# Optimization experiments

Measured on AMD Instinct MI355X. Metric: run time of the kernel, lower is better.

Reference implementation:

```python
import jax, jax.numpy as jnp
import numpy as np
import math
from jax import lax

B, L_IN, D_MODEL = 128, 1000, 384
SEQ = 250          # AdaptiveMaxPool1d target length
NHEAD, NL = 8, 4
HID = 342          # convolution_hidden_dim
NUM_CLASSES = 10
FACTOR = 5         # ProbAttention factor


def _ln(x, w, b, eps=1e-5):
    mu = x.mean(-1, keepdims=True)
    var = ((x - mu) ** 2).mean(-1, keepdims=True)
    return (x - mu) * lax.rsqrt(var + eps) * w + b


def _conv1d(x, w, b, groups):
    # x: [B,C,L], w: [O, I/groups, K], SAME padding (padding=1 for k=3)
    y = lax.conv_general_dilated(x, w, (1,), 'SAME',
                                 dimension_numbers=('NCH', 'OIH', 'NCH'),
                                 feature_group_count=groups)
    return y + b[None, :, None]


def _prob_attention(x, Wq, bq, Wk, bk, Wv, bv, Wo, bo, key):
    # Informer-style ProbSparse attention, mask_flag=False, eval mode (no dropout)
    Bs, L, d = x.shape
    H, Dh = NHEAD, d // NHEAD
    q = (x @ Wq + bq).reshape(Bs, L, H, Dh).transpose(0, 2, 1, 3)  # [B,H,L,Dh]
    k = (x @ Wk + bk).reshape(Bs, L, H, Dh).transpose(0, 2, 1, 3)
    v = (x @ Wv + bv).reshape(Bs, L, H, Dh).transpose(0, 2, 1, 3)
    U = min(int(FACTOR * math.ceil(math.log(L))), L)  # sampled keys per query (=30)
    u = min(int(FACTOR * math.ceil(math.log(L))), L)  # top queries kept (=30)
    idx = jax.random.randint(key, (L, U), 0, L)        # shared key sample per query row
    k_samp = k[:, :, idx, :]                            # [B,H,L,U,Dh] gather
    qk_samp = jnp.einsum('bhld,bhlud->bhlu', q, k_samp)
    M = qk_samp.max(-1) - qk_samp.mean(-1)              # sparsity measure [B,H,L]
    top = lax.top_k(M, u)[1]                            # [B,H,u]
    q_red = jnp.take_along_axis(q, top[..., None], axis=2)          # [B,H,u,Dh]
    scores = jnp.einsum('bhud,bhld->bhul', q_red, k) / math.sqrt(Dh)
    attn = jax.nn.softmax(scores, axis=-1)
    ctx_top = jnp.einsum('bhul,bhld->bhud', attn, v)                # [B,H,u,Dh]
    # initial context = mean of V (mask_flag=False); scatter top-query contexts
    ctx = jnp.broadcast_to(v.mean(2, keepdims=True), (Bs, H, L, Dh))
    bi = jnp.arange(Bs)[:, None, None]
    hi = jnp.arange(H)[None, :, None]
    ctx = ctx.at[bi, hi, top].set(ctx_top)
    out = ctx.transpose(0, 2, 1, 3).reshape(Bs, L, d)
    return out @ Wo + bo


def _forward(x, pos_embed, ln_in_w, ln_in_b, lnA_w, lnA_b, Wq, bq, Wk, bk, Wv, bv,
             Wo, bo, lnB_w, lnB_b, c1a_w, c1a_b, c1b_w, c1b_b, lnC_w, lnC_b,
             c2_w, c2_b, ln2_w, ln2_b, fc_w, fc_b):
    Bs, Lin, d = x.shape
    # AdaptiveMaxPool1d(250): Lin=1000 is an exact multiple -> window-4 max
    x = x.reshape(Bs, SEQ, Lin // SEQ, d).max(axis=2)
    x = _ln(x, ln_in_w, ln_in_b)
    x = x + pos_embed[:, :SEQ, :]                       # positional embedding (dropout off)
    for l in range(NL):
        key = jax.random.fold_in(jax.random.key(42), l)
        # residual 1: LN -> ProbSparse attention
        h = _ln(x, lnA_w[l], lnA_b[l])
        x = x + _prob_attention(h, Wq[l], bq[l], Wk[l], bk[l], Wv[l], bv[l],
                                Wo[l], bo[l], key)
        # residual 2: LN -> grouped conv over sequence axis (channels = d_model)
        h = _ln(x, lnB_w[l], lnB_b[l]).transpose(0, 2, 1)  # [B,d,L]
        h = jax.nn.gelu(_conv1d(h, c1a_w[l], c1a_b[l], 3))
        h = _conv1d(h, c1b_w[l], c1b_b[l], 3)
        x = x + h.transpose(0, 2, 1)
        # residual 3: LN -> grouped conv treating sequence (250) as channels
        h = _ln(x, lnC_w[l], lnC_b[l])                     # [B,250,d]
        h = jax.nn.gelu(_conv1d(h, c2_w[l], c2_b[l], 2))
        x = x + h
    x = _ln(x, ln2_w, ln2_b)
    x = x.max(axis=1)                                   # AdaptiveMaxPool1d(1)
    x = _ln(x, ln2_w, ln2_b)                            # LN2 reused, per original
    return x @ fc_w + fc_b


def setup_inputs() -> dict:
    key = jax.random.key(0)
    ks = jax.random.split(key, 12)
    s = 0.02
    f32 = jnp.float32
    inp = {
        'x': jax.random.normal(ks[0], (B, L_IN, D_MODEL), f32),
        'pos_embed': jax.random.normal(ks[1], (1, 1500, D_MODEL), f32) * s,
        'ln_in_w': jnp.ones((D_MODEL,), f32), 'ln_in_b': jnp.zeros((D_MODEL,), f32),
        'lnA_w': jnp.ones((NL, D_MODEL), f32), 'lnA_b': jnp.zeros((NL, D_MODEL), f32),
        'Wq': jax.random.normal(ks[2], (NL, D_MODEL, D_MODEL), f32) * s,
        'bq': jnp.zeros((NL, D_MODEL), f32),
        'Wk': jax.random.normal(ks[3], (NL, D_MODEL, D_MODEL), f32) * s,
        'bk': jnp.zeros((NL, D_MODEL), f32),
        'Wv': jax.random.normal(ks[4], (NL, D_MODEL, D_MODEL), f32) * s,
        'bv': jnp.zeros((NL, D_MODEL), f32),
        'Wo': jax.random.normal(ks[5], (NL, D_MODEL, D_MODEL), f32) * s,
        'bo': jnp.zeros((NL, D_MODEL), f32),
        'lnB_w': jnp.ones((NL, D_MODEL), f32), 'lnB_b': jnp.zeros((NL, D_MODEL), f32),
        'c1a_w': jax.random.normal(ks[6], (NL, HID, D_MODEL // 3, 3), f32) * s,
        'c1a_b': jnp.zeros((NL, HID), f32),
        'c1b_w': jax.random.normal(ks[7], (NL, D_MODEL, HID // 3, 3), f32) * s,
        'c1b_b': jnp.zeros((NL, D_MODEL), f32),
        'lnC_w': jnp.ones((NL, D_MODEL), f32), 'lnC_b': jnp.zeros((NL, D_MODEL), f32),
        'c2_w': jax.random.normal(ks[8], (NL, SEQ, SEQ // 2, 3), f32) * s,
        'c2_b': jnp.zeros((NL, SEQ), f32),
        'ln2_w': jnp.ones((D_MODEL,), f32), 'ln2_b': jnp.zeros((D_MODEL,), f32),
        'fc_w': jax.random.normal(ks[9], (D_MODEL, NUM_CLASSES), f32) * s,
        'fc_b': jnp.zeros((NUM_CLASSES,), f32),
    }
    return inp


def reference(x, pos_embed, ln_in_w, ln_in_b, lnA_w, lnA_b, Wq, bq, Wk, bk, Wv, bv,
              Wo, bo, lnB_w, lnB_b, c1a_w, c1a_b, c1b_w, c1b_b, lnC_w, lnC_b,
              c2_w, c2_b, ln2_w, ln2_b, fc_w, fc_b):
    return _forward(x, pos_embed, ln_in_w, ln_in_b, lnA_w, lnA_b, Wq, bq, Wk, bk,
                    Wv, bv, Wo, bo, lnB_w, lnB_b, c1a_w, c1a_b, c1b_w, c1b_b,
                    lnC_w, lnC_b, c2_w, c2_b, ln2_w, ln2_b, fc_w, fc_b)
```

## Files before the change

### kernel.cpp

```cpp
#include <hip/hip_runtime.h>
#include <hip/hip_bf16.h>
#include <cfloat>
#include <cstdint>

static constexpr int Bb   = 128;
static constexpr int SEQ  = 250;
static constexpr int DM   = 384;
static constexpr int NH   = 8;
static constexpr int DHd  = 48;
static constexpr int HID  = 342;
static constexpr int UU   = 30;

using bf16 = __hip_bfloat16;
typedef __attribute__((ext_vector_type(8))) short bf16x8;
typedef __attribute__((ext_vector_type(4))) float f32x4;

__device__ __forceinline__ float unpk_lo(uint32_t p){ return __builtin_bit_cast(float, p << 16); }
__device__ __forceinline__ float unpk_hi(uint32_t p){ return __builtin_bit_cast(float, p & 0xffff0000u); }

__device__ __forceinline__ int swz_st(int lane){ return (((lane & 7) ^ (lane >> 3)) << 3); }
__device__ __forceinline__ int swz_rd(int ks, int lane){ return ((((ks<<2) + (lane >> 4)) ^ (lane & 7)) << 3); }

__device__ __forceinline__ int xcd_swz(int orig, int nwg){
  int q = nwg >> 3, r = nwg & 7;
  int x = orig & 7, i = orig >> 3;
  int start = (x < r) ? x*(q+1) : r*(q+1) + (x-r)*q;
  return start + i;
}

__device__ __forceinline__ uint32_t rotl32(uint32_t x, int n){ return (x<<n)|(x>>(32-n)); }
#define TF_R(x0,x1,r) { x0 += x1; x1 = rotl32(x1,(r)); x1 ^= x0; }
__device__ inline void threefry(uint32_t k0, uint32_t k1, uint32_t x0, uint32_t x1,
                                uint32_t &o0, uint32_t &o1){
  uint32_t ks2 = k0 ^ k1 ^ 0x1BD11BDAu;
  x0 += k0; x1 += k1;
  TF_R(x0,x1,13) TF_R(x0,x1,15) TF_R(x0,x1,26) TF_R(x0,x1,6)
  x0 += k1; x1 += ks2 + 1u;
  TF_R(x0,x1,17) TF_R(x0,x1,29) TF_R(x0,x1,16) TF_R(x0,x1,24)
  x0 += ks2; x1 += k0 + 2u;
  TF_R(x0,x1,13) TF_R(x0,x1,15) TF_R(x0,x1,26) TF_R(x0,x1,6)
  x0 += k0; x1 += k1 + 3u;
  TF_R(x0,x1,17) TF_R(x0,x1,29) TF_R(x0,x1,16) TF_R(x0,x1,24)
  x0 += k1; x1 += ks2 + 4u;
  TF_R(x0,x1,13) TF_R(x0,x1,15) TF_R(x0,x1,26) TF_R(x0,x1,6)
  x0 += ks2; x1 += k0 + 5u;
  o0 = x0; o1 = x1;
}

__global__ void idx_kernel(int* __restrict__ IDX){
  int i = blockIdx.x*256 + threadIdx.x;
  if (i >= 4*7500) return;
  int l = i / 7500;
  int t = i % 7500;
  uint32_t fk0, fk1;
  threefry(0u, 42u, 0u, (uint32_t)l, fk0, fk1);
  uint32_t a0,a1,b0,b1;
  threefry(fk0, fk1, 0u, 2u, a0, a1);
  threefry(fk0, fk1, 1u, 3u, b0, b1);
  uint32_t c0 = (t < 3750) ? (uint32_t)t          : (uint32_t)(t-3750);
  uint32_t c1 = (t < 3750) ? (uint32_t)(t+3750)   : (uint32_t)t;
  uint32_t y0, y1, hi, lo;
  threefry(a0, b0, c0, c1, y0, y1); hi = (t < 3750) ? y0 : y1;
  threefry(a1, b1, c0, c1, y0, y1); lo = (t < 3750) ? y0 : y1;
  uint32_t val = ((hi % 250u) * 46u + (lo % 250u)) % 250u;
  IDX[i] = (int)val;
}

__device__ __forceinline__ float block_sum(float v, float* red){
  v += __shfl_down(v,32); v += __shfl_down(v,16); v += __shfl_down(v,8);
  v += __shfl_down(v,4);  v += __shfl_down(v,2);  v += __shfl_down(v,1);
  int lane = threadIdx.x & 63, wid = threadIdx.x >> 6, nw = blockDim.x >> 6;
  __syncthreads();
  if (lane == 0) red[wid] = v;
  __syncthreads();
  float r = red[0];
  for (int i=1;i<nw;i++) r += red[i];
  return r;
}

__device__ __forceinline__ float gelu_tanh(float x){
  float t = 0.7978845608028654f * (x + 0.044715f * x * x * x);
  return 0.5f * x * (1.f + tanhf(t));
}

__global__ __launch_bounds__(384) void pool_ln_pos(const float* __restrict__ xin,
    const float* __restrict__ pos, const float* __restrict__ w, const float* __restrict__ b,
    float* __restrict__ X){
  __shared__ float red[8];
  int bs = blockIdx.x; int bb = bs / SEQ, s = bs % SEQ; int d = threadIdx.x;
  const float* xp = xin + ((size_t)bb*1000 + (size_t)s*4)*DM + d;
  float v = fmaxf(fmaxf(xp[0], xp[DM]), fmaxf(xp[2*DM], xp[3*DM]));
  float mu = block_sum(v, red) * (1.f/DM);
  float diff = v - mu;
  float var = block_sum(diff*diff, red) * (1.f/DM);
  X[(size_t)bs*DM + d] = diff * rsqrtf(var + 1e-5f) * w[d] + b[d] + pos[(size_t)s*DM + d];
}

template<int MODE>
__global__ __launch_bounds__(256) void ln_wave(const float* __restrict__ in,
    float* __restrict__ o32, bf16* __restrict__ o16, bf16* __restrict__ olo,
    const float* __restrict__ w, const float* __restrict__ b){
  size_t row = (size_t)blockIdx.x*4 + (threadIdx.x >> 6);
  int lane = threadIdx.x & 63;
  const float* rp = in + row*DM;
  float v[6];
  #pragma unroll
  for (int i = 0; i < 6; i++) v[i] = rp[lane + 64*i];
  float s = v[0]+v[1]+v[2]+v[3]+v[4]+v[5];
  #pragma unroll
  for (int off = 32; off; off >>= 1) s += __shfl_xor(s, off);
  float mu = s * (1.f/DM);
  float q = 0.f;
  #pragma unroll
  for (int i = 0; i < 6; i++){ float d = v[i]-mu; q += d*d; }
  #pragma unroll
  for (int off = 32; off; off >>= 1) q += __shfl_xor(q, off);
  float rs = rsqrtf(q*(1.f/DM) + 1e-5f);
  #pragma unroll
  for (int i = 0; i < 6; i++){
    int d = lane + 64*i;
    float y = (v[i]-mu)*rs*w[d] + b[d];
    if (MODE == 0) o32[row*DM + d] = y;
    if (MODE == 1) o16[row*DM + d] = __float2bfloat16(y);
    if (MODE == 2){
      bf16 h = __float2bfloat16(y);
      o16[row*DM + d] = h;
      olo[row*DM + d] = __float2bfloat16(y - __bfloat162float(h));
    }
  }
}

__device__ __forceinline__ void gload16(const void* g, void* l){
  __builtin_amdgcn_global_load_lds(
      (__attribute__((address_space(1))) void*)(g),
      (__attribute__((address_space(3))) void*)(l), 16, 0, 0);
}

template<int EPI>
__global__ __launch_bounds__(256) void mfma_gemm(
    const bf16* __restrict__ A, const bf16* __restrict__ WT,
    const float* __restrict__ bias, float* __restrict__ Cf, bf16* __restrict__ Cb,
    const bf16* __restrict__ zpage)
{
  __shared__ bf16 As[128*64];
  __shared__ bf16 Bs[128*64];
  const int tid = threadIdx.x;
  const int wid = tid >> 6, lane = tid & 63;
  const int wr = wid >> 1, wc = wid & 1;
  const int wg = xcd_swz(blockIdx.x, 750);
  const int bm = (wg / 3) * 128;
  const int bn = (wg % 3) * 128;
  const int srow = lane >> 3;
  const int scolz = swz_st(lane);

  f32x4 acc[4][4] = {};
  for (int ck = 0; ck < 6; ck++){
    const int kk0 = ck * 64;
    __syncthreads();
    #pragma unroll
    for (int s = 0; s < 4; s++){
      int row = wid*32 + s*8 + srow;
      gload16(A + (size_t)(bm + row)*DM + kk0 + scolz, &As[(wid*32 + s*8)*64]);
    }
    #pragma unroll
    for (int s = 0; s < 4; s++){
      int row = wid*32 + s*8 + srow;
      gload16(WT + (size_t)(bn + row)*DM + kk0 + scolz, &Bs[(wid*32 + s*8)*64]);
    }
    __syncthreads();
    #pragma unroll
    for (int ks = 0; ks < 2; ks++){
      const int fo = swz_rd(ks, lane);
      bf16x8 af[4], bg[4];
      #pragma unroll
      for (int m = 0; m < 4; m++)
        af[m] = *(const bf16x8*)&As[(wr*64 + m*16 + (lane & 15))*64 + fo];
      #pragma unroll
      for (int n = 0; n < 4; n++)
        bg[n] = *(const bf16x8*)&Bs[(wc*64 + n*16 + (lane & 15))*64 + fo];
      #pragma unroll
      for (int m = 0; m < 4; m++)
        #pragma unroll
        for (int n = 0; n < 4; n++)
          acc[m][n] = __builtin_amdgcn_mfma_f32_16x16x32_bf16(af[m], bg[n], acc[m][n], 0, 0, 0);
    }
  }
  const int c_l = lane & 15, r4 = (lane >> 4) * 4;
  #pragma unroll
  for (int m = 0; m < 4; m++){
    #pragma unroll
    for (int n = 0; n < 4; n++){
      #pragma unroll
      for (int r = 0; r < 4; r++){
        int token = bm + wr*64 + m*16 + r4 + r;
        int col   = bn + wc*64 + n*16 + c_l;
        float v = acc[m][n][r] + bias[col];
        if (EPI == 0)      Cf[(size_t)token*DM + col] = v;
        else if (EPI == 1) Cf[(size_t)token*DM + col] += v;
        else if (EPI == 2) Cb[(size_t)token*DM + col] = __float2bfloat16(gelu_tanh(v));
        else               Cb[(size_t)token*DM + col] = __float2bfloat16(v);
      }
    }
  }
}

template<int EPI, int KIN>
__global__ __launch_bounds__(256) void mfma_c1g(
    const bf16* __restrict__ A, const bf16* __restrict__ WG,
    const float* __restrict__ bias, float* __restrict__ Cf, bf16* __restrict__ Cb,
    const bf16* __restrict__ zpage)
{
  __shared__ bf16 As[128*64];
  __shared__ bf16 Bs[128*64];
  const int tid = threadIdx.x;
  const int wid = tid >> 6, lane = tid & 63;
  const int wr = wid >> 1, wc = wid & 1;
  const int wg = xcd_swz(blockIdx.x, 750);
  const int bm = (wg / 3) * 128;
  const int g  = wg % 3;
  const int srow = lane >> 3;
  const int scolz = swz_st(lane);

  f32x4 acc[4][4] = {};
  for (int ck = 0; ck < 6; ck++){
    const int tap = ck >> 1;
    const int kk0 = (ck & 1) * 64;
    __syncthreads();
    #pragma unroll
    for (int s = 0; s < 4; s++){
      int row = wid*32 + s*8 + srow;
      int token = bm + row;
      int l = token - (token/SEQ)*SEQ;
      int ls = l + tap - 1;
      bool valid = (ls >= 0) && (ls < SEQ);
      const bf16* src = valid ? (A + (size_t)(token + tap - 1)*DM + g*KIN + kk0 + scolz) : zpage;
      gload16(src, &As[(wid*32 + s*8)*64]);
    }
    #pragma unroll
    for (int s = 0; s < 4; s++){
      int row = wid*32 + s*8 + srow;
      gload16(WG + ((size_t)(g*3 + tap)*128 + row)*128 + kk0 + scolz, &Bs[(wid*32 + s*8)*64]);
    }
    __syncthreads();
    #pragma unroll
    for (int ks = 0; ks < 2; ks++){
      const int fo = swz_rd(ks, lane);
      bf16x8 af[4], bg[4];
      #pragma unroll
      for (int m = 0; m < 4; m++)
        af[m] = *(const bf16x8*)&As[(wr*64 + m*16 + (lane & 15))*64 + fo];
      #pragma unroll
      for (int n = 0; n < 4; n++)
        bg[n] = *(const bf16x8*)&Bs[(wc*64 + n*16 + (lane & 15))*64 + fo];
      #pragma unroll
      for (int m = 0; m < 4; m++)
        #pragma unroll
        for (int n = 0; n < 4; n++)
          acc[m][n] = __builtin_amdgcn_mfma_f32_16x16x32_bf16(af[m], bg[n], acc[m][n], 0, 0, 0);
    }
  }
  const int c_l = lane & 15, r4 = (lane >> 4) * 4;
  #pragma unroll
  for (int m = 0; m < 4; m++){
    #pragma unroll
    for (int n = 0; n < 4; n++){
      #pragma unroll
      for (int r = 0; r < 4; r++){
        int token = bm + wr*64 + m*16 + r4 + r;
        int cl    = wc*64 + n*16 + c_l;
        if (EPI == 2){
          if (cl < 114){
            int col = g*114 + cl;
            float v = acc[m][n][r] + bias[col];
            Cb[(size_t)token*DM + col] = __float2bfloat16(gelu_tanh(v));
          }
        } else {
          int col = g*128 + cl;
          float v = acc[m][n][r] + bias[col];
          Cf[(size_t)token*DM + col] += v;
        }
      }
    }
  }
}

__global__ __launch_bounds__(256) void mfma_qk2(
    const bf16* __restrict__ Ahi, const bf16* __restrict__ Alo,
    const bf16* __restrict__ WqT, const bf16* __restrict__ WkT,
    const float* __restrict__ bq, const float* __restrict__ bk,
    bf16* __restrict__ Qhi, bf16* __restrict__ Qlo,
    bf16* __restrict__ Khi, bf16* __restrict__ Klo)
{
  __shared__ bf16 As[128*64];
  __shared__ bf16 BsQ[64*64];
  __shared__ bf16 BsK[64*64];
  const int tid = threadIdx.x;
  const int wid = tid >> 6, lane = tid & 63;
  const int wr = wid >> 1, wc = wid & 1;
  const int wg = xcd_swz(blockIdx.x, 1500);
  const int bm = (wg / 6) * 128;
  const int bn = (wg % 6) * 64;
  const int srow = lane >> 3;
  const int scolz = swz_st(lane);

  f32x4 accQ[4][2] = {};
  f32x4 accK[4][2] = {};
  for (int kk6 = 0; kk6 < 6; kk6++){
    const int kk0 = kk6 * 64;
    for (int p = 0; p < 3; p++){
      const size_t wo = (p == 1) ? (size_t)DM*DM : 0;
      __syncthreads();
      if (p != 1){
        const bf16* Asrc = (p == 0) ? Ahi : Alo;
        #pragma unroll
        for (int s = 0; s < 4; s++){
          int row = wid*32 + s*8 + srow;
          gload16(Asrc + (size_t)(bm + row)*DM + kk0 + scolz, &As[(wid*32 + s*8)*64]);
        }
      }
      #pragma unroll
      for (int s = 0; s < 2; s++){
        int row = wid*16 + s*8 + srow;
        gload16(WqT + wo + (size_t)(bn + row)*DM + kk0 + scolz, &BsQ[(wid*16 + s*8)*64]);
        gload16(WkT + wo + (size_t)(bn + row)*DM + kk0 + scolz, &BsK[(wid*16 + s*8)*64]);
      }
      __syncthreads();
      #pragma unroll
      for (int ks = 0; ks < 2; ks++){
        const int fo = swz_rd(ks, lane);
        bf16x8 af[4], bgq[2], bgk[2];
        #pragma unroll
        for (int m = 0; m < 4; m++)
          af[m] = *(const bf16x8*)&As[(wr*64 + m*16 + (lane & 15))*64 + fo];
        #pragma unroll
        for (int n = 0; n < 2; n++){
          bgq[n] = *(const bf16x8*)&BsQ[(wc*32 + n*16 + (lane & 15))*64 + fo];
          bgk[n] = *(const bf16x8*)&BsK[(wc*32 + n*16 + (lane & 15))*64 + fo];
        }
        #pragma unroll
        for (int m = 0; m < 4; m++)
          #pragma unroll
          for (int n = 0; n < 2; n++){
            accQ[m][n] = __builtin_amdgcn_mfma_f32_16x16x32_bf16(af[m], bgq[n], accQ[m][n], 0, 0, 0);
            accK[m][n] = __builtin_amdgcn_mfma_f32_16x16x32_bf16(af[m], bgk[n], accK[m][n], 0, 0, 0);
          }
      }
    }
  }
  const int c_l = lane & 15, r4 = (lane >> 4) * 4;
  #pragma unroll
  for (int m = 0; m < 4; m++)
    #pragma unroll
    for (int n = 0; n < 2; n++)
      #pragma unroll
      for (int r = 0; r < 4; r++){
        int token = bm + wr*64 + m*16 + r4 + r;
        int col   = bn + wc*32 + n*16 + c_l;
        size_t off = (size_t)token*DM + col;
        float qv = accQ[m][n][r] + bq[col];
        float kv = accK[m][n][r] + bk[col];
        bf16 qh = __float2bfloat16(qv);
        bf16 kh = __float2bfloat16(kv);
        Qhi[off] = qh; Qlo[off] = __float2bfloat16(qv - __bfloat162float(qh));
        Khi[off] = kh; Klo[off] = __float2bfloat16(kv - __bfloat162float(kh));
      }
}

__global__ __launch_bounds__(256) void conv2_mfma(
    const bf16* __restrict__ HT, const bf16* __restrict__ W2T,
    const float* __restrict__ bias, float* __restrict__ X,
    const bf16* __restrict__ zpage)
{
  __shared__ bf16 As[128*64];
  __shared__ bf16 Bs[128*64];
  const int tid = threadIdx.x;
  const int wid = tid >> 6, lane = tid & 63;
  const int wr = wid >> 1, wc = wid & 1;
  const int wg = xcd_swz(blockIdx.x, 768);
  const int bn = (wg % 3) * 128;
  const int g  = (wg / 3) & 1;
  const int b  = wg / 6;
  const int srow = lane >> 3;
  const int scolz = swz_st(lane);
  const bf16* Wbase = W2T + (size_t)g*3*128*128;

  f32x4 acc[4][4] = {};
  for (int ck = 0; ck < 6; ck++){
    const int tap = ck >> 1;
    const int kk0 = (ck & 1) * 64;
    __syncthreads();
    #pragma unroll
    for (int s = 0; s < 4; s++){
      gload16(Wbase + ((size_t)tap*128 + wid*32 + s*8 + srow)*128 + kk0 + scolz, &As[(wid*32 + s*8)*64]);
    }
    #pragma unroll
    for (int s = 0; s < 4; s++){
      int row = wid*32 + s*8 + srow;
      int sd = bn + row + tap - 1;
      const bf16* src = (sd >= 0 && sd < DM)
        ? (HT + (((size_t)b*DM + sd)*2 + g)*128 + kk0 + scolz) : zpage;
      gload16(src, &Bs[(wid*32 + s*8)*64]);
    }
    __syncthreads();
    #pragma unroll
    for (int ks = 0; ks < 2; ks++){
      const int fo = swz_rd(ks, lane);
      bf16x8 af[4], bg[4];
      #pragma unroll
      for (int m = 0; m < 4; m++)
        af[m] = *(const bf16x8*)&As[(wr*64 + m*16 + (lane & 15))*64 + fo];
      #pragma unroll
      for (int n = 0; n < 4; n++)
        bg[n] = *(const bf16x8*)&Bs[(wc*64 + n*16 + (lane & 15))*64 + fo];
      #pragma unroll
      for (int m = 0; m < 4; m++)
        #pragma unroll
        for (int n = 0; n < 4; n++)
          acc[m][n] = __builtin_amdgcn_mfma_f32_16x16x32_bf16(af[m], bg[n], acc[m][n], 0, 0, 0);
    }
  }
  const int c_l = lane & 15, r4 = (lane >> 4) * 4;
  #pragma unroll
  for (int m = 0; m < 4; m++){
    #pragma unroll
    for (int n = 0; n < 4; n++){
      #pragma unroll
      for (int r = 0; r < 4; r++){
        int lo = wr*64 + m*16 + r4 + r;
        if (lo < 125){
          int d = bn + wc*64 + n*16 + c_l;
          float v = acc[m][n][r] + bias[g*125 + lo];
          X[((size_t)b*SEQ + g*125 + lo)*DM + d] += gelu_tanh(v);
        }
      }
    }
  }
}

__global__ __launch_bounds__(256) void transpose_ht(const bf16* __restrict__ H,
                                                    bf16* __restrict__ HT){
  __shared__ bf16 t[68][66];
  int d0 = blockIdx.x * 64;
  int p0 = blockIdx.y * 64;
  int b  = blockIdx.z;
  int tid = threadIdx.x;
  int l0 = p0 - 3;
  for (int i = tid; i < 68*64; i += 256){
    int r = i >> 6, c = i & 63;
    int l = l0 + r;
    bf16 v = __float2bfloat16(0.f);
    if (l >= 0 && l < SEQ) v = H[((size_t)b*SEQ + l)*DM + d0 + c];
    t[r][c] = v;
  }
  __syncthreads();
  for (int i = tid; i < 64*64; i += 256){
    int rr = i >> 6, cc = i & 63;
    int p = p0 + cc;
    int gg = p >> 7, li = p & 127;
    int l = gg*125 + li;
    bf16 v = __float2bfloat16(0.f);
    if (li < 125 && l < SEQ) v = t[l - l0][rr];
    HT[((size_t)b*DM + d0 + rr)*256 + p] = v;
  }
}

__global__ void zfill(bf16* z){ z[threadIdx.x] = __float2bfloat16(0.f); }

__global__ __launch_bounds__(256) void build_projT(const float* __restrict__ Wv,
    const float* __restrict__ Wo, bf16* __restrict__ WvT, bf16* __restrict__ WoT){
  __shared__ float t[32][33];
  int mat = blockIdx.z;
  const float* W = (mat < 4) ? (Wv + (size_t)mat*DM*DM) : (Wo + (size_t)(mat-4)*DM*DM);
  bf16* WT = (mat < 4) ? (WvT + (size_t)mat*DM*DM) : (WoT + (size_t)(mat-4)*DM*DM);
  int k0 = blockIdx.y*32, n0 = blockIdx.x*32;
  int tx = threadIdx.x & 31, ty = threadIdx.x >> 5;
  #pragma unroll
  for (int r = 0; r < 32; r += 8)
    t[ty + r][tx] = W[(size_t)(k0 + ty + r)*DM + n0 + tx];
  __syncthreads();
  #pragma unroll
  for (int r = 0; r < 32; r += 8)
    WT[(size_t)(n0 + ty + r)*DM + k0 + tx] = __float2bfloat16(t[tx][ty + r]);
}

__global__ __launch_bounds__(256) void build_qkhl(const float* __restrict__ Wq,
    const float* __restrict__ Wk, bf16* __restrict__ WT){
  __shared__ float t[32][33];
  int mat = blockIdx.z;
  const float* W = (mat < 4) ? (Wq + (size_t)mat*DM*DM) : (Wk + (size_t)(mat-4)*DM*DM);
  bf16* hi = WT + (size_t)mat*2*DM*DM;
  bf16* lo = hi + (size_t)DM*DM;
  int k0 = blockIdx.y*32, n0 = blockIdx.x*32;
  int tx = threadIdx.x & 31, ty = threadIdx.x >> 5;
  #pragma unroll
  for (int r = 0; r < 32; r += 8)
    t[ty + r][tx] = W[(size_t)(k0 + ty + r)*DM + n0 + tx];
  __syncthreads();
  #pragma unroll
  for (int r = 0; r < 32; r += 8){
    float w = t[tx][ty + r];
    bf16 h = __float2bfloat16(w);
    hi[(size_t)(n0 + ty + r)*DM + k0 + tx] = h;
    lo[(size_t)(n0 + ty + r)*DM + k0 + tx] = __float2bfloat16(w - __bfloat162float(h));
  }
}

__global__ void build_biasA(const float* __restrict__ bin, float* __restrict__ bias_pad){
  int i = blockIdx.x*256 + threadIdx.x;
  if (i >= 4*DM) return;
  int l = i/DM, n = i%DM;
  bias_pad[i] = (n < HID) ? bin[l*HID + n] : 0.f;
}

__global__ void build_c1aG(const float* __restrict__ W, bf16* __restrict__ WG){
  int i = blockIdx.x*256 + threadIdx.x;
  if (i >= 4*3*3*128*128) return;
  int k   = i & 127;
  int n   = (i >> 7) & 127;
  int tap = (i / 16384) % 3;
  int g   = (i / 49152) % 3;
  int l   = i / 147456;
  float v = 0.f;
  if (n < 114)
    v = W[(((size_t)l*HID + g*114 + n)*128 + k)*3 + tap];
  WG[i] = __float2bfloat16(v);
}

__global__ void build_c1bG(const float* __restrict__ W, bf16* __restrict__ WG){
  int i = blockIdx.x*256 + threadIdx.x;
  if (i >= 4*3*3*128*128) return;
  int k   = i & 127;
  int n   = (i >> 7) & 127;
  int tap = (i / 16384) % 3;
  int g   = (i / 49152) % 3;
  int l   = i / 147456;
  float v = 0.f;
  if (k < 114)
    v = W[(((size_t)l*DM + g*128 + n)*114 + k)*3 + tap];
  WG[i] = __float2bfloat16(v);
}

__global__ void build_c2T(const float* __restrict__ W, bf16* __restrict__ WT){
  int i = blockIdx.x*256 + threadIdx.x;
  if (i >= 4*2*3*128*128) return;
  int li = i & 127;
  int lo = (i >> 7) & 127;
  int t  = (i / 16384) % 3;
  int g  = (i / 49152) % 2;
  int l  = i / 98304;
  float v = 0.f;
  if (lo < 125 && li < 125)
    v = W[(((size_t)l*SEQ + g*125 + lo)*125 + li)*3 + t];
  WT[i] = __float2bfloat16(v);
}

__global__ __launch_bounds__(256) void probe_mfma(
    const bf16* __restrict__ Qhi, const bf16* __restrict__ Qlo,
    const bf16* __restrict__ Khi, const bf16* __restrict__ Klo,
    const int* __restrict__ idx, int* __restrict__ TOP,
    const bf16* __restrict__ zpage)
{
  __shared__ bf16  Qsh[32*64];
  __shared__ bf16  Qsl[32*64];
  __shared__ float Ssh[32*257];
  __shared__ int   IDXsh[32*UU];
  __shared__ float Msh[256];
  __shared__ float s_redv[4];
  __shared__ int   s_redi[4];
  __shared__ int   s_win;
  const int bh = xcd_swz(blockIdx.x, Bb*NH);
  const int h = bh & 7; const int b = bh >> 3;
  const int tid = threadIdx.x;
  const int wid = tid >> 6, lane = tid & 63;
  const int scolz = swz_st(lane);
  const size_t qkbase = (size_t)(b*SEQ)*DM + h*DHd;

  bf16x8 kfh[4][2] = {};
  bf16x8 kfl[4][2] = {};
  {
    const int colb = wid*64 + (lane & 15);
    const int kb   = (lane >> 4) * 8;
    #pragma unroll
    for (int n = 0; n < 4; n++){
      int col = colb + n*16;
      int cc  = (col < SEQ) ? col : (SEQ-1);
      const bf16* ph = Khi + qkbase + (size_t)cc*DM;
      const bf16* pl = Klo + qkbase + (size_t)cc*DM;
      kfh[n][0] = *(const bf16x8*)(ph + kb);
      kfl[n][0] = *(const bf16x8*)(pl + kb);
      if (kb + 32 < DHd){
        kfh[n][1] = *(const bf16x8*)(ph + kb + 32);
        kfl[n][1] = *(const bf16x8*)(pl + kb + 32);
      }
    }
  }

  const int c_l = lane & 15, r4 = (lane >> 4) * 4;
  for (int t = 0; t < 8; t++){
    const int r0 = t*32;
    {
      int row = r0 + wid*8 + (lane >> 3);
      bool v = (row < SEQ) && (scolz < DHd);
      const bf16* sh = v ? (Qhi + qkbase + (size_t)row*DM + scolz) : zpage;
      const bf16* sl = v ? (Qlo + qkbase + (size_t)row*DM + scolz) : zpage;
      gload16(sh, &Qsh[(wid*8)*64]);
      gload16(sl, &Qsl[(wid*8)*64]);
    }
    for (int i = tid; i < 32*UU; i += 256){
      int r = i / UU;
      int row = r0 + r;
      IDXsh[i] = (row < SEQ) ? idx[row*UU + (i - r*UU)] : 0;
    }
    __syncthreads();
    f32x4 acc[2][4] = {};
    #pragma unroll
    for (int p = 0; p < 3; p++){
      const bf16* A = (p < 2) ? Qsh : Qsl;
      #pragma unroll
      for (int ks = 0; ks < 2; ks++){
        const int fo = swz_rd(ks, lane);
        bf16x8 af[2];
        #pragma unroll
        for (int m = 0; m < 2; m++)
          af[m] = *(const bf16x8*)&A[(m*16 + (lane & 15))*64 + fo];
        #pragma unroll
        for (int m = 0; m < 2; m++)
          #pragma unroll
          for (int n = 0; n < 4; n++){
            bf16x8 bg = (p == 1) ? kfl[n][ks] : kfh[n][ks];
            acc[m][n] = __builtin_amdgcn_mfma_f32_16x16x32_bf16(af[m], bg, acc[m][n], 0, 0, 0);
          }
      }
    }
    #pragma unroll
    for (int m = 0; m < 2; m++)
      #pragma unroll
      for (int n = 0; n < 4; n++)
        #pragma unroll
        for (int r = 0; r < 4; r++)
          Ssh[(m*16 + r4 + r)*257 + wid*64 + n*16 + c_l] = acc[m][n][r];
    __syncthreads();
    {
      int rl = tid >> 3, s8 = tid & 7;
      int row = r0 + rl;
      float mx = -FLT_MAX, sm = 0.f;
      #pragma unroll
      for (int uu = 0; uu < 4; uu++){
        int u = s8 + uu*8;
        if (u < UU){
          int c = IDXsh[rl*UU + u];
          float v = Ssh[rl*257 + c];
          mx = fmaxf(mx, v); sm += v;
        }
      }
      #pragma unroll
      for (int off = 4; off; off >>= 1){
        mx = fmaxf(mx, __shfl_xor(mx, off));
        sm += __shfl_xor(sm, off);
      }
      if (s8 == 0 && row < SEQ) Msh[row] = mx - sm*(1.f/UU);
    }
    __syncthreads();
  }
  float Mv  = (tid < SEQ) ? Msh[tid] : -FLT_MAX;
  int  myid = (tid < SEQ) ? tid : (1<<30);
  for (int sel = 0; sel < UU; sel++){
    float bv = Mv; int bi = myid;
    #pragma unroll
    for (int off = 32; off; off >>= 1){
      float ov = __shfl_xor(bv, off);
      int   oi = __shfl_xor(bi, off);
      if (ov > bv || (ov == bv && oi < bi)){ bv = ov; bi = oi; }
    }
    if (lane == 0){ s_redv[wid] = bv; s_redi[wid] = bi; }
    __syncthreads();
    if (tid == 0){
      float wv = s_redv[0]; int wi = s_redi[0];
      #pragma unroll
      for (int q = 1; q < 4; q++)
        if (s_redv[q] > wv || (s_redv[q] == wv && s_redi[q] < wi)){ wv = s_redv[q]; wi = s_redi[q]; }
      TOP[(size_t)bh*UU + sel] = wi;
      s_win = wi;
    }
    __syncthreads();
    if (myid == s_win) Mv = -FLT_MAX;
  }
}

static constexpr int SSTR = 260;
static constexpr int VSTR = 132;
__global__ __launch_bounds__(256) void attn_ctx5(
    const bf16* __restrict__ Qhi, const bf16* __restrict__ Qlo,
    const bf16* __restrict__ Khi, const bf16* __restrict__ Klo,
    const bf16* __restrict__ V16,
    const int* __restrict__ TOP, bf16* __restrict__ CTX,
    const bf16* __restrict__ zpage)
{
  __shared__ bf16  Qt[32*64];
  __shared__ bf16  Qtl[32*64];
  __shared__ float Ssh[32*SSTR];
  __shared__ uint32_t Vsh[DHd*VSTR];
  __shared__ float vpart[5][DHd];
  __shared__ float vmean[DHd];
  __shared__ float invsh[32];
  __shared__ int   TOPsh[32];
  __shared__ int   mark[SEQ];
  const int bh = xcd_swz(blockIdx.x, Bb*NH);
  const int h = bh & 7; const int b = bh >> 3;
  const int tid = threadIdx.x;
  const int wid = tid >> 6, lane = tid & 63;
  const int scolz = swz_st(lane);
  const size_t base = (size_t)(b*SEQ)*DM + h*DHd;

  bf16x8 kfh[4][2] = {};
  bf16x8 kfl[4][2] = {};
  {
    const int colb = wid*64 + (lane & 15);
    const int kb   = (lane >> 4) * 8;
    #pragma unroll
    for (int n = 0; n < 4; n++){
      int col = colb + n*16;
      int cc  = (col < SEQ) ? col : (SEQ-1);
      const bf16* ph = Khi + base + (size_t)cc*DM;
      const bf16* pl = Klo + base + (size_t)cc*DM;
      kfh[n][0] = *(const bf16x8*)(ph + kb);
      kfl[n][0] = *(const bf16x8*)(pl + kb);
      if (kb + 32 < DHd){
        kfh[n][1] = *(const bf16x8*)(ph + kb + 32);
        kfl[n][1] = *(const bf16x8*)(pl + kb + 32);
      }
    }
  }
  if (tid < UU) TOPsh[tid] = TOP[(size_t)bh*UU + tid];
  for (int i = tid; i < SEQ; i += 256) mark[i] = -1;
  const uint16_t* vp16 = (const uint16_t*)(V16 + base);
  for (int i = tid; i < DHd*128; i += 256){
    int dh = i >> 7, jp = i & 127;
    uint32_t v = 0;
    if (jp < 125){
      uint32_t a = vp16[(size_t)(2*jp)*DM + dh];
      uint32_t c = vp16[(size_t)(2*jp+1)*DM + dh];
      v = a | (c << 16);
    }
    Vsh[dh*VSTR + jp] = v;
  }
  {
    int row = wid*8 + (lane >> 3);
    bool v = (row < UU) && (scolz < DHd);
    int tr = v ? TOP[(size_t)bh*UU + row] : 0;
    const bf16* sh = v ? (Qhi + base + (size_t)tr*DM + scolz) : zpage;
    const bf16* sl = v ? (Qlo + base + (size_t)tr*DM + scolz) : zpage;
    gload16(sh, &Qt[(wid*8)*64]);
    gload16(sl, &Qtl[(wid*8)*64]);
  }
  __syncthreads();
  if (tid < UU) mark[TOPsh[tid]] = tid;

  const int c_l = lane & 15, r4 = (lane >> 4) * 4;
  {
    f32x4 acc[2][4] = {};
    #pragma unroll
    for (int p = 0; p < 3; p++){
      const bf16* A = (p < 2) ? Qt : Qtl;
      #pragma unroll
      for (int ks = 0; ks < 2; ks++){
        const int fo = swz_rd(ks, lane);
        bf16x8 af[2];
        #pragma unroll
        for (int m = 0; m < 2; m++)
          af[m] = *(const bf16x8*)&A[(m*16 + (lane & 15))*64 + fo];
        #pragma unroll
        for (int m = 0; m < 2; m++)
          #pragma unroll
          for (int n = 0; n < 4; n++){
            bf16x8 bg = (p == 1) ? kfl[n][ks] : kfh[n][ks];
            acc[m][n] = __builtin_amdgcn_mfma_f32_16x16x32_bf16(af[m], bg, acc[m][n], 0, 0, 0);
          }
      }
    }
    #pragma unroll
    for (int m = 0; m < 2; m++)
      #pragma unroll
      for (int n = 0; n < 4; n++)
        #pragma unroll
        for (int r = 0; r < 4; r++)
          Ssh[(m*16 + r4 + r)*SSTR + wid*64 + n*16 + c_l] = acc[m][n][r];
  }
  __syncthreads();

  {
    const float scale = 0.14433756729740643f;
    for (int rr = 0; rr < 8; rr++){
      int row = wid*8 + rr;
      float* Sr = &Ssh[row*SSTR];
      if (row < UU){
        float xs[4];
        #pragma unroll
        for (int j = 0; j < 4; j++){
          int c = lane + 64*j;
          xs[j] = (c < SEQ) ? Sr[c]*scale : -FLT_MAX;
        }
        float mx = fmaxf(fmaxf(xs[0],xs[1]), fmaxf(xs[2],xs[3]));
        #pragma unroll
        for (int off = 32; off; off >>= 1) mx = fmaxf(mx, __shfl_xor(mx, off));
        float sm = 0.f;
        #pragma unroll
        for (int j = 0; j < 4; j++){
          int c = lane + 64*j;
          float e = (c < SEQ) ? expf(xs[j]-mx) : 0.f;
          Sr[c] = e;
          sm += e;
        }
        #pragma unroll
        for (int off = 32; off; off >>= 1) sm += __shfl_xor(sm, off);
        if (lane == 0) invsh[row] = 1.f/sm;
      } else {
        #pragma unroll
        for (int j = 0; j < 4; j++) Sr[lane + 64*j] = 0.f;
      }
    }
    if (tid < 240){
      int dh = tid % DHd, pr = tid / DHd;
      const uint32_t* vr = &Vsh[dh*VSTR + pr*25];
      float s = 0.f;
      #pragma unroll
      for (int z = 0; z < 25; z++){ uint32_t vp = vr[z]; s += unpk_lo(vp) + unpk_hi(vp); }
      vpart[pr][dh] = s;
    }
  }
  __syncthreads();
  if (tid < DHd)
    vmean[tid] = (vpart[0][tid]+vpart[1][tid]+vpart[2][tid]+vpart[3][tid]+vpart[4][tid]) * (1.f/SEQ);

  if (wid < 3){
    const int dh0 = wid*16;
    f32x4 acc2[2] = {};
    for (int kc = 0; kc < 8; kc++){
      bf16x8 bv = *(const bf16x8*)&Vsh[(dh0 + (lane & 15))*VSTR + kc*16 + (lane >> 4)*4];
      #pragma unroll
      for (int m = 0; m < 2; m++){
        const float* pr = &Ssh[(m*16 + (lane & 15))*SSTR + kc*32 + (lane >> 4)*8];
        bf16x8 pa;
        #pragma unroll
        for (int i = 0; i < 8; i++){
          bf16 hh = __float2bfloat16(pr[i]);
          pa[i] = *reinterpret_cast<short*>(&hh);
        }
        acc2[m] = __builtin_amdgcn_mfma_f32_16x16x32_bf16(pa, bv, acc2[m], 0, 0, 0);
      }
    }
    #pragma unroll
    for (int m = 0; m < 2; m++)
      #pragma unroll
      for (int r = 0; r < 4; r++){
        int u = m*16 + r4 + r;
        if (u < UU){
          float val = acc2[m][r] * invsh[u];
          CTX[(size_t)(b*SEQ + TOPsh[u])*DM + h*DHd + dh0 + c_l] = __float2bfloat16(val);
        }
      }
  }
  __syncthreads();
  for (int i = tid; i < SEQ*DHd; i += 256){
    int l = i / DHd, dh = i - l*DHd;
    if (mark[l] < 0)
      CTX[(size_t)(b*SEQ + l)*DM + h*DHd + dh] = __float2bfloat16(vmean[dh]);
  }
}

__global__ __launch_bounds__(384) void final_kernel(const float* __restrict__ Hin,
    const float* __restrict__ w, const float* __restrict__ bparm,
    const float* __restrict__ fcw, const float* __restrict__ fcb, float* __restrict__ out){
  __shared__ float red[8];
  __shared__ float ybuf[DM];
  int b = blockIdx.x; int d = threadIdx.x;
  const float* hp = Hin + (size_t)b*SEQ*DM + d;
  float mx = -FLT_MAX;
  for (int l=0;l<SEQ;l++) mx = fmaxf(mx, hp[(size_t)l*DM]);
  float mu = block_sum(mx, red) * (1.f/DM);
  float diff = mx - mu;
  float var = block_sum(diff*diff, red) * (1.f/DM);
  float y = diff * rsqrtf(var + 1e-5f) * w[d] + bparm[d];
  ybuf[d] = y;
  __syncthreads();
  if (d < 10){
    float acc = fcb[d];
    for (int k=0;k<DM;k++) acc += ybuf[k] * fcw[k*10 + d];
    out[b*10 + d] = acc;
  }
}

extern "C" void kernel_launch(void* const* d_in, const int* in_sizes, int n_in,
                              void* d_out, int out_size, void* d_ws, size_t ws_size,
                              hipStream_t stream) {
  const float* x     = (const float*)d_in[0];
  const float* pos   = (const float*)d_in[1];
  const float* lniw  = (const float*)d_in[2];
  const float* lnib  = (const float*)d_in[3];
  const float* lnAw  = (const float*)d_in[4];
  const float* lnAb  = (const float*)d_in[5];
  const float* Wq    = (const float*)d_in[6];
  const float* bq    = (const float*)d_in[7];
  const float* Wk    = (const float*)d_in[8];
  const float* bk    = (const float*)d_in[9];
  const float* Wv    = (const float*)d_in[10];
  const float* bv    = (const float*)d_in[11];
  const float* Wo    = (const float*)d_in[12];
  const float* bo    = (const float*)d_in[13];
  const float* lnBw  = (const float*)d_in[14];
  const float* lnBb  = (const float*)d_in[15];
  const float* c1aw  = (const float*)d_in[16];
  const float* c1ab  = (const float*)d_in[17];
  const float* c1bw  = (const float*)d_in[18];
  const float* c1bb  = (const float*)d_in[19];
  const float* lnCw  = (const float*)d_in[20];
  const float* lnCb  = (const float*)d_in[21];
  const float* c2w   = (const float*)d_in[22];
  const float* c2b   = (const float*)d_in[23];
  const float* ln2w  = (const float*)d_in[24];
  const float* ln2b  = (const float*)d_in[25];
  const float* fcw   = (const float*)d_in[26];
  const float* fcb   = (const float*)d_in[27];
  float* out = (float*)d_out;

  const size_t ACT  = (size_t)Bb*SEQ*DM;
  float* Xb  = (float*)d_ws;
  float* Hb  = Xb  + ACT;
  float* Qb  = Hb  + ACT;
  float* Kb  = Qb  + ACT;
  float* Vb  = Kb  + ACT;
  float* biasA = Vb + ACT;
  int*   TOP = (int*)(biasA + 4*DM);
  int*   IDX = TOP + (size_t)Bb*NH*UU;
  bf16*  Hb16 = (bf16*)(IDX + 4*7500);
  bf16*  G1   = Hb16 + ACT;
  bf16*  WvT  = G1   + ACT;
  bf16*  WoT  = WvT  + (size_t)4*DM*DM;
  bf16*  WaG  = WoT  + (size_t)4*DM*DM;
  bf16*  WbG  = WaG  + (size_t)12*DM*DM;
  bf16*  WqkT = WbG  + (size_t)12*DM*DM;
  bf16*  W2T  = WqkT + (size_t)16*DM*DM;
  bf16*  zp   = W2T  + (size_t)4*2*3*128*128;

  bf16* Qhi = (bf16*)Qb; bf16* Qlo = Qhi + ACT;
  bf16* Khi = (bf16*)Kb; bf16* Klo = Khi + ACT;
  bf16* V16 = (bf16*)Vb;

  zfill<<<dim3(1), dim3(256), 0, stream>>>(zp);
  hipMemsetAsync(G1, 0, ACT*sizeof(bf16), stream);
  idx_kernel<<<dim3(118), dim3(256), 0, stream>>>(IDX);
  build_projT<<<dim3(12,12,8), dim3(256), 0, stream>>>(Wv, Wo, WvT, WoT);
  build_qkhl<<<dim3(12,12,8), dim3(256), 0, stream>>>(Wq, Wk, WqkT);
  build_biasA<<<dim3(6), dim3(256), 0, stream>>>(c1ab, biasA);
  build_c1aG<<<dim3(2304), dim3(256), 0, stream>>>(c1aw, WaG);
  build_c1bG<<<dim3(2304), dim3(256), 0, stream>>>(c1bw, WbG);
  build_c2T<<<dim3(1536), dim3(256), 0, stream>>>(c2w, W2T);
  pool_ln_pos<<<dim3(32000), dim3(384), 0, stream>>>(x, pos, lniw, lnib, Xb);

  for (int l = 0; l < 4; l++){
    const size_t wofs = (size_t)l*DM*DM;
    bf16* Alo16 = (bf16*)Hb;
    bf16* CTX16 = Hb16;
    bf16* HTb   = (bf16*)Qb;
    ln_wave<2><<<dim3(8000), dim3(256), 0, stream>>>(Xb, (float*)nullptr, Hb16, Alo16, lnAw + l*DM, lnAb + l*DM);
    mfma_qk2<<<dim3(1500), dim3(256), 0, stream>>>(Hb16, Alo16,
        WqkT + (size_t)l*2*DM*DM, WqkT + (size_t)(4+l)*2*DM*DM,
        bq + l*DM, bk + l*DM, Qhi, Qlo, Khi, Klo);
    mfma_gemm<3><<<dim3(750), dim3(256), 0, stream>>>(Hb16, WvT + wofs, bv + l*DM, (float*)nullptr, V16, zp);
    probe_mfma<<<dim3(Bb*NH), dim3(256), 0, stream>>>(Qhi, Qlo, Khi, Klo, IDX + l*7500, TOP, zp);
    attn_ctx5<<<dim3(Bb*NH), dim3(256), 0, stream>>>(Qhi, Qlo, Khi, Klo, V16, TOP, CTX16, zp);
    mfma_gemm<1><<<dim3(750), dim3(256), 0, stream>>>(CTX16, WoT + wofs, bo + l*DM, Xb, (bf16*)nullptr, zp);

    ln_wave<1><<<dim3(8000), dim3(256), 0, stream>>>(Xb, (float*)nullptr, Hb16, (bf16*)nullptr, lnBw + l*DM, lnBb + l*DM);
    mfma_c1g<2,128><<<dim3(750), dim3(256), 0, stream>>>(Hb16, WaG + (size_t)l*3*3*128*128, biasA + l*DM, (float*)nullptr, G1, zp);
    mfma_c1g<1,114><<<dim3(750), dim3(256), 0, stream>>>(G1, WbG + (size_t)l*3*3*128*128, c1bb + l*DM, Xb, (bf16*)nullptr, zp);

    ln_wave<1><<<dim3(8000), dim3(256), 0, stream>>>(Xb, (float*)nullptr, Hb16, (bf16*)nullptr, lnCw + l*DM, lnCb + l*DM);
    transpose_ht<<<dim3(6,4,Bb), dim3(256), 0, stream>>>(Hb16, HTb);
    conv2_mfma<<<dim3(768), dim3(256), 0, stream>>>(HTb, W2T + (size_t)l*2*3*128*128, c2b + l*SEQ, Xb, zp);
  }

  ln_wave<0><<<dim3(8000), dim3(256), 0, stream>>>(Xb, Hb, (bf16*)nullptr, (bf16*)nullptr, ln2w, ln2b);
  final_kernel<<<dim3(Bb), dim3(384), 0, stream>>>(Hb, ln2w, ln2b, fcw, fcb, out);
}
```

Before: 2.222 ms.

## Fuse ProbSparse probe/top-k kernel into attention context kernel

```diff
diff --git a/kernel.cpp b/kernel.cpp
--- a/kernel.cpp
+++ b/kernel.cpp
@@ -554,156 +554,27 @@
   WT[i] = __float2bfloat16(v);
 }
 
-__global__ __launch_bounds__(256) void probe_mfma(
+static constexpr int SSTR = 260;
+static constexpr int VSTR = 132;
+__global__ __launch_bounds__(256) void attn_fused(
     const bf16* __restrict__ Qhi, const bf16* __restrict__ Qlo,
     const bf16* __restrict__ Khi, const bf16* __restrict__ Klo,
-    const int* __restrict__ idx, int* __restrict__ TOP,
-    const bf16* __restrict__ zpage)
+    const bf16* __restrict__ V16, const int* __restrict__ idx,
+    bf16* __restrict__ CTX, const bf16* __restrict__ zpage)
 {
   __shared__ bf16  Qsh[32*64];
   __shared__ bf16  Qsl[32*64];
-  __shared__ float Ssh[32*257];
+  __shared__ float Ssh[32*SSTR];
+  __shared__ uint32_t Vsh[DHd*VSTR];
   __shared__ int   IDXsh[32*UU];
   __shared__ float Msh[256];
   __shared__ float s_redv[4];
   __shared__ int   s_redi[4];
   __shared__ int   s_win;
-  const int bh = xcd_swz(blockIdx.x, Bb*NH);
-  const int h = bh & 7; const int b = bh >> 3;
-  const int tid = threadIdx.x;
-  const int wid = tid >> 6, lane = tid & 63;
-  const int scolz = swz_st(lane);
-  const size_t qkbase = (size_t)(b*SEQ)*DM + h*DHd;
-
-  bf16x8 kfh[4][2] = {};
-  bf16x8 kfl[4][2] = {};
-  {
-    const int colb = wid*64 + (lane & 15);
-    const int kb   = (lane >> 4) * 8;
-    #pragma unroll
-    for (int n = 0; n < 4; n++){
-      int col = colb + n*16;
-      int cc  = (col < SEQ) ? col : (SEQ-1);
-      const bf16* ph = Khi + qkbase + (size_t)cc*DM;
-      const bf16* pl = Klo + qkbase + (size_t)cc*DM;
-      kfh[n][0] = *(const bf16x8*)(ph + kb);
-      kfl[n][0] = *(const bf16x8*)(pl + kb);
-      if (kb + 32 < DHd){
-        kfh[n][1] = *(const bf16x8*)(ph + kb + 32);
-        kfl[n][1] = *(const bf16x8*)(pl + kb + 32);
-      }
-    }
-  }
-
-  const int c_l = lane & 15, r4 = (lane >> 4) * 4;
-  for (int t = 0; t < 8; t++){
-    const int r0 = t*32;
-    {
-      int row = r0 + wid*8 + (lane >> 3);
-      bool v = (row < SEQ) && (scolz < DHd);
-      const bf16* sh = v ? (Qhi + qkbase + (size_t)row*DM + scolz) : zpage;
-      const bf16* sl = v ? (Qlo + qkbase + (size_t)row*DM + scolz) : zpage;
-      gload16(sh, &Qsh[(wid*8)*64]);
-      gload16(sl, &Qsl[(wid*8)*64]);
-    }
-    for (int i = tid; i < 32*UU; i += 256){
-      int r = i / UU;
-      int row = r0 + r;
-      IDXsh[i] = (row < SEQ) ? idx[row*UU + (i - r*UU)] : 0;
-    }
-    __syncthreads();
-    f32x4 acc[2][4] = {};
-    #pragma unroll
-    for (int p = 0; p < 3; p++){
-      const bf16* A = (p < 2) ? Qsh : Qsl;
-      #pragma unroll
-      for (int ks = 0; ks < 2; ks++){
-        const int fo = swz_rd(ks, lane);
-        bf16x8 af[2];
-        #pragma unroll
-        for (int m = 0; m < 2; m++)
-          af[m] = *(const bf16x8*)&A[(m*16 + (lane & 15))*64 + fo];
-        #pragma unroll
-        for (int m = 0; m < 2; m++)
-          #pragma unroll
-          for (int n = 0; n < 4; n++){
-            bf16x8 bg = (p == 1) ? kfl[n][ks] : kfh[n][ks];
-            acc[m][n] = __builtin_amdgcn_mfma_f32_16x16x32_bf16(af[m], bg, acc[m][n], 0, 0, 0);
-          }
-      }
-    }
-    #pragma unroll
-    for (int m = 0; m < 2; m++)
-      #pragma unroll
-      for (int n = 0; n < 4; n++)
-        #pragma unroll
-        for (int r = 0; r < 4; r++)
-          Ssh[(m*16 + r4 + r)*257 + wid*64 + n*16 + c_l] = acc[m][n][r];
-    __syncthreads();
-    {
-      int rl = tid >> 3, s8 = tid & 7;
-      int row = r0 + rl;
-      float mx = -FLT_MAX, sm = 0.f;
-      #pragma unroll
-      for (int uu = 0; uu < 4; uu++){
-        int u = s8 + uu*8;
-        if (u < UU){
-          int c = IDXsh[rl*UU + u];
-          float v = Ssh[rl*257 + c];
-          mx = fmaxf(mx, v); sm += v;
-        }
-      }
-      #pragma unroll
-      for (int off = 4; off; off >>= 1){
-        mx = fmaxf(mx, __shfl_xor(mx, off));
-        sm += __shfl_xor(sm, off);
-      }
-      if (s8 == 0 && row < SEQ) Msh[row] = mx - sm*(1.f/UU);
-    }
-    __syncthreads();
-  }
-  float Mv  = (tid < SEQ) ? Msh[tid] : -FLT_MAX;
-  int  myid = (tid < SEQ) ? tid : (1<<30);
-  for (int sel = 0; sel < UU; sel++){
-    float bv = Mv; int bi = myid;
-    #pragma unroll
-    for (int off = 32; off; off >>= 1){
-      float ov = __shfl_xor(bv, off);
-      int   oi = __shfl_xor(bi, off);
-      if (ov > bv || (ov == bv && oi < bi)){ bv = ov; bi = oi; }
-    }
-    if (lane == 0){ s_redv[wid] = bv; s_redi[wid] = bi; }
-    __syncthreads();
-    if (tid == 0){
-      float wv = s_redv[0]; int wi = s_redi[0];
-      #pragma unroll
-      for (int q = 1; q < 4; q++)
-        if (s_redv[q] > wv || (s_redv[q] == wv && s_redi[q] < wi)){ wv = s_redv[q]; wi = s_redi[q]; }
-      TOP[(size_t)bh*UU + sel] = wi;
-      s_win = wi;
-    }
-    __syncthreads();
-    if (myid == s_win) Mv = -FLT_MAX;
-  }
-}
-
-static constexpr int SSTR = 260;
-static constexpr int VSTR = 132;
-__global__ __launch_bounds__(256) void attn_ctx5(
-    const bf16* __restrict__ Qhi, const bf16* __restrict__ Qlo,
-    const bf16* __restrict__ Khi, const bf16* __restrict__ Klo,
-    const bf16* __restrict__ V16,
-    const int* __restrict__ TOP, bf16* __restrict__ CTX,
-    const bf16* __restrict__ zpage)
-{
-  __shared__ bf16  Qt[32*64];
-  __shared__ bf16  Qtl[32*64];
-  __shared__ float Ssh[32*SSTR];
-  __shared__ uint32_t Vsh[DHd*VSTR];
+  __shared__ int   TOPsh[32];
+  __shared__ float invsh[32];
   __shared__ float vpart[5][DHd];
   __shared__ float vmean[DHd];
-  __shared__ float invsh[32];
-  __shared__ int   TOPsh[32];
   __shared__ int   mark[SEQ];
   const int bh = xcd_swz(blockIdx.x, Bb*NH);
   const int h = bh & 7; const int b = bh >> 3;
@@ -731,8 +602,6 @@
       }
     }
   }
-  if (tid < UU) TOPsh[tid] = TOP[(size_t)bh*UU + tid];
-  for (int i = tid; i < SEQ; i += 256) mark[i] = -1;
   const uint16_t* vp16 = (const uint16_t*)(V16 + base);
   for (int i = tid; i < DHd*128; i += 256){
     int dh = i >> 7, jp = i & 127;
@@ -744,24 +613,29 @@
     }
     Vsh[dh*VSTR + jp] = v;
   }
-  {
-    int row = wid*8 + (lane >> 3);
-    bool v = (row < UU) && (scolz < DHd);
-    int tr = v ? TOP[(size_t)bh*UU + row] : 0;
-    const bf16* sh = v ? (Qhi + base + (size_t)tr*DM + scolz) : zpage;
-    const bf16* sl = v ? (Qlo + base + (size_t)tr*DM + scolz) : zpage;
-    gload16(sh, &Qt[(wid*8)*64]);
-    gload16(sl, &Qtl[(wid*8)*64]);
-  }
-  __syncthreads();
-  if (tid < UU) mark[TOPsh[tid]] = tid;
+  for (int i = tid; i < SEQ; i += 256) mark[i] = -1;
 
   const int c_l = lane & 15, r4 = (lane >> 4) * 4;
-  {
+  for (int t = 0; t < 8; t++){
+    const int r0 = t*32;
+    {
+      int row = r0 + wid*8 + (lane >> 3);
+      bool v = (row < SEQ) && (scolz < DHd);
+      const bf16* sh = v ? (Qhi + base + (size_t)row*DM + scolz) : zpage;
+      const bf16* sl = v ? (Qlo + base + (size_t)row*DM + scolz) : zpage;
+      gload16(sh, &Qsh[(wid*8)*64]);
+      gload16(sl, &Qsl[(wid*8)*64]);
+    }
+    for (int i = tid; i < 32*UU; i += 256){
+      int r = i / UU;
+      int row = r0 + r;
+      IDXsh[i] = (row < SEQ) ? idx[row*UU + (i - r*UU)] : 0;
+    }
+    __syncthreads();
     f32x4 acc[2][4] = {};
     #pragma unroll
     for (int p = 0; p < 3; p++){
-      const bf16* A = (p < 2) ? Qt : Qtl;
+      const bf16* A = (p < 2) ? Qsh : Qsl;
       #pragma unroll
       for (int ks = 0; ks < 2; ks++){
         const int fo = swz_rd(ks, lane);
@@ -785,9 +659,95 @@
         #pragma unroll
         for (int r = 0; r < 4; r++)
           Ssh[(m*16 + r4 + r)*SSTR + wid*64 + n*16 + c_l] = acc[m][n][r];
-  }
-  __syncthreads();
-
+    __syncthreads();
+    {
+      int rl = tid >> 3, s8 = tid & 7;
+      int row = r0 + rl;
+      float mx = -FLT_MAX, sm = 0.f;
+      #pragma unroll
+      for (int uu = 0; uu < 4; uu++){
+        int u = s8 + uu*8;
+        if (u < UU){
+          int c = IDXsh[rl*UU + u];
+          float v = Ssh[rl*SSTR + c];
+          mx = fmaxf(mx, v); sm += v;
+        }
+      }
+      #pragma unroll
+      for (int off = 4; off; off >>= 1){
+        mx = fmaxf(mx, __shfl_xor(mx, off));
+        sm += __shfl_xor(sm, off);
+      }
+      if (s8 == 0 && row < SEQ) Msh[row] = mx - sm*(1.f/UU);
+    }
+    __syncthreads();
+  }
+  float Mv  = (tid < SEQ) ? Msh[tid] : -FLT_MAX;
+  int  myid = (tid < SEQ) ? tid : (1<<30);
+  for (int sel = 0; sel < UU; sel++){
+    float bv = Mv; int bi = myid;
+    #pragma unroll
+    for (int off = 32; off; off >>= 1){
+      float ov = __shfl_xor(bv, off);
+      int   oi = __shfl_xor(bi, off);
+      if (ov > bv || (ov == bv && oi < bi)){ bv = ov; bi = oi; }
+    }
+    if (lane == 0){ s_redv[wid] = bv; s_redi[wid] = bi; }
+    __syncthreads();
+    if (tid == 0){
+      float wv = s_redv[0]; int wi = s_redi[0];
+      #pragma unroll
+      for (int q = 1; q < 4; q++)
+        if (s_redv[q] > wv || (s_redv[q] == wv && s_redi[q] < wi)){ wv = s_redv[q]; wi = s_redi[q]; }
+      TOPsh[sel] = wi;
+      s_win = wi;
+    }
+    __syncthreads();
+    if (myid == s_win) Mv = -FLT_MAX;
+  }
+  __syncthreads();
+  if (tid < UU) mark[TOPsh[tid]] = tid;
+
+  {
+    int row = wid*8 + (lane >> 3);
+    bool v = (row < UU) && (scolz < DHd);
+    int tr = v ? TOPsh[row] : 0;
+    const bf16* sh = v ? (Qhi + base + (size_t)tr*DM + scolz) : zpage;
+    const bf16* sl = v ? (Qlo + base + (size_t)tr*DM + scolz) : zpage;
+    gload16(sh, &Qsh[(wid*8)*64]);
+    gload16(sl, &Qsl[(wid*8)*64]);
+  }
+  __syncthreads();
+  {
+    f32x4 acc[2][4] = {};
+    #pragma unroll
+    for (int p = 0; p < 3; p++){
+      const bf16* A = (p < 2) ? Qsh : Qsl;
+      #pragma unroll
+      for (int ks = 0; ks < 2; ks++){
+        const int fo = swz_rd(ks, lane);
+        bf16x8 af[2];
+        #pragma unroll
+        for (int m = 0; m < 2; m++)
+          af[m] = *(const bf16x8*)&A[(m*16 + (lane & 15))*64 + fo];
+        #pragma unroll
+        for (int m = 0; m < 2; m++)
+          #pragma unroll
+          for (int n = 0; n < 4; n++){
+            bf16x8 bg = (p == 1) ? kfl[n][ks] : kfh[n][ks];
+            acc[m][n] = __builtin_amdgcn_mfma_f32_16x16x32_bf16(af[m], bg, acc[m][n], 0, 0, 0);
+          }
+      }
+    }
+    #pragma unroll
+    for (int m = 0; m < 2; m++)
+      #pragma unroll
+      for (int n = 0; n < 4; n++)
+        #pragma unroll
+        for (int r = 0; r < 4; r++)
+          Ssh[(m*16 + r4 + r)*SSTR + wid*64 + n*16 + c_l] = acc[m][n][r];
+  }
+  __syncthreads();
   {
     const float scale = 0.14433756729740643f;
     for (int rr = 0; rr < 8; rr++){
@@ -967,8 +927,7 @@
         WqkT + (size_t)l*2*DM*DM, WqkT + (size_t)(4+l)*2*DM*DM,
         bq + l*DM, bk + l*DM, Qhi, Qlo, Khi, Klo);
     mfma_gemm<3><<<dim3(750), dim3(256), 0, stream>>>(Hb16, WvT + wofs, bv + l*DM, (float*)nullptr, V16, zp);
-    probe_mfma<<<dim3(Bb*NH), dim3(256), 0, stream>>>(Qhi, Qlo, Khi, Klo, IDX + l*7500, TOP, zp);
-    attn_ctx5<<<dim3(Bb*NH), dim3(256), 0, stream>>>(Qhi, Qlo, Khi, Klo, V16, TOP, CTX16, zp);
+    attn_fused<<<dim3(Bb*NH), dim3(256), 0, stream>>>(Qhi, Qlo, Khi, Klo, V16, IDX + l*7500, CTX16, zp);
     mfma_gemm<1><<<dim3(750), dim3(256), 0, stream>>>(CTX16, WoT + wofs, bo + l*DM, Xb, (bf16*)nullptr, zp);
 
     ln_wave<1><<<dim3(8000), dim3(256), 0, stream>>>(Xb, (float*)nullptr, Hb16, (bf16*)nullptr, lnBw + l*DM, lnBb + l*DM);
```

New measurement: 2.159 ms. -2.8%, faster.
